# Optimization experiments

Hardware: AMD Instinct MI355X
Metric: run time of the kernel (lower is better)

## Reference

```python
import jax, jax.numpy as jnp
import numpy as np

B, S, H = 8, 2048, 256

def setup_inputs() -> dict:
    key = jax.random.key(0)
    ks = jax.random.split(key, 6)
    scale = 1.0 / np.sqrt(H)
    return {
        "query": jax.random.normal(ks[0], (B, S, H), dtype=jnp.float32),
        "key_in": jax.random.normal(ks[1], (B, S, H), dtype=jnp.float32),
        "value": jax.random.normal(ks[2], (B, S, H), dtype=jnp.float32),
        "Wq": jax.random.uniform(ks[3], (H, H), dtype=jnp.float32, minval=-scale, maxval=scale),
        "Wk": jax.random.uniform(ks[4], (H, H), dtype=jnp.float32, minval=-scale, maxval=scale),
        "Wv": jax.random.uniform(ks[5], (H, H), dtype=jnp.float32, minval=-scale, maxval=scale),
    }

def reference(query, key_in, value, Wq, Wk, Wv):
    # nn.Linear(bias=False): y = x @ W.T
    q = jnp.einsum('bsh,dh->bsd', query, Wq)
    k = jnp.einsum('bsh,dh->bsd', key_in, Wk)
    v = jnp.einsum('bsh,dh->bsd', value, Wv)
    # unscaled attention, exactly as in the torch module
    scores = jnp.einsum('bqd,bkd->bqk', q, k)  # [B, Sq, Skv]
    weights = jax.nn.softmax(scores, axis=-1)
    context = jnp.einsum('bqk,bkd->bqd', weights, v)
    return context
```

## Files before the change

kernel.cpp:

```cpp
#include <hip/hip_runtime.h>
#include <hip/hip_bf16.h>

typedef short short8 __attribute__((ext_vector_type(8)));
typedef _Float16 half8 __attribute__((ext_vector_type(8)));
typedef __fp16 fp16x2 __attribute__((ext_vector_type(2)));
typedef float f32x4  __attribute__((ext_vector_type(4)));
typedef float f32x16 __attribute__((ext_vector_type(16)));

__device__ __forceinline__ unsigned short f2h(float f) {
  _Float16 h = (_Float16)f;
  return __builtin_bit_cast(unsigned short, h);
}
__device__ __forceinline__ half8 as_h8(short8 s) { return __builtin_bit_cast(half8, s); }

__global__ __launch_bounds__(256) void proj_kernel(
    const float* __restrict__ Aq, const float* __restrict__ Bq,
    const float* __restrict__ Ak, const float* __restrict__ Bk,
    const float* __restrict__ Av, const float* __restrict__ Bv,
    short* __restrict__ Cq, short* __restrict__ Ck, short* __restrict__ Cv) {
  __shared__ short At[128][40];
  __shared__ short Bt[128][40];
  const int y = blockIdx.y;
  const float* A  = (y == 0) ? Aq : (y == 1) ? Ak : Av;
  const float* Bm = (y == 0) ? Bq : (y == 1) ? Bk : Bv;
  short* C        = (y == 0) ? Cq : (y == 1) ? Ck : Cv;
  const int mode = (y == 2);
  const float scale = (y == 0) ? 1.44269504f : 1.0f;
  const int x = blockIdx.x;
  const int batch = x & 7, loc = (x >> 3) & 15, half = x >> 7;
  int m0, n0;
  if (!mode) { m0 = (batch * 16 + loc) * 128; n0 = half * 128; }
  else       { m0 = half * 128; n0 = (batch * 16 + loc) * 128; }

  const int t = threadIdx.x;
  const int w = t >> 6, l = t & 63;
  const int wr = (w >> 1) * 64, wc = (w & 1) * 64;
  f32x4 acc[4][4] = {};
  for (int k0 = 0; k0 < 256; k0 += 32) {
    __syncthreads();
    #pragma unroll
    for (int rep = 0; rep < 4; ++rep) {
      int row = (t >> 3) + rep * 32;
      int c4  = (t & 7) * 4;
      float4 va = *(const float4*)(A + (size_t)(m0 + row) * 256 + k0 + c4);
      unsigned long long pa = (unsigned long long)f2h(va.x) |
                              ((unsigned long long)f2h(va.y) << 16) |
                              ((unsigned long long)f2h(va.z) << 32) |
                              ((unsigned long long)f2h(va.w) << 48);
      *(unsigned long long*)&At[row][c4] = pa;
      float4 vb = *(const float4*)(Bm + (size_t)(n0 + row) * 256 + k0 + c4);
      unsigned long long pb = (unsigned long long)f2h(vb.x) |
                              ((unsigned long long)f2h(vb.y) << 16) |
                              ((unsigned long long)f2h(vb.z) << 32) |
                              ((unsigned long long)f2h(vb.w) << 48);
      *(unsigned long long*)&Bt[row][c4] = pb;
    }
    __syncthreads();
    short8 af[4], bf[4];
    #pragma unroll
    for (int i = 0; i < 4; ++i) {
      af[i] = *(const short8*)&At[wr + i * 16 + (l & 15)][(l >> 4) * 8];
      bf[i] = *(const short8*)&Bt[wc + i * 16 + (l & 15)][(l >> 4) * 8];
    }
    #pragma unroll
    for (int i = 0; i < 4; ++i)
      #pragma unroll
      for (int j = 0; j < 4; ++j)
        acc[i][j] = __builtin_amdgcn_mfma_f32_16x16x32_f16(as_h8(af[i]), as_h8(bf[j]),
                                                           acc[i][j], 0, 0, 0);
  }
  #pragma unroll
  for (int i = 0; i < 4; ++i)
    #pragma unroll
    for (int j = 0; j < 4; ++j)
      #pragma unroll
      for (int r = 0; r < 4; ++r) {
        int row = m0 + wr + i * 16 + (l >> 4) * 4 + r;
        int col = n0 + wc + j * 16 + (l & 15);
        size_t idx;
        if (!mode) {
          int b = row >> 11, s = row & 2047;
          int T = s >> 5, ln = s & 31;
          int kf = col >> 4, g = (col >> 3) & 1, jj = col & 7;
          idx = (((size_t)(b * 64 + T) * 16 + kf) * 64 + g * 32 + ln) * 8 + jj;
        } else {
          int b = col >> 11, s = col & 2047;
          int T = s >> 5, k2 = (s >> 4) & 1, g = (s >> 3) & 1, jj = s & 7;
          int db = row >> 5, ln = row & 31;
          idx = ((((size_t)(b * 64 + T) * 2 + k2) * 8 + db) * 64 + g * 32 + ln) * 8 + jj;
        }
        C[idx] = (short)f2h(acc[i][j][r] * scale);
      }
}

__global__ __launch_bounds__(512, 4) void attn_kernel(const short* __restrict__ QP,
                                                      const short* __restrict__ KP,
                                                      const short* __restrict__ VP,
                                                      float* __restrict__ O) {
  __shared__ __align__(16) char arena[16384 + 40960 + 1024 + 1024];
  short* Qlds = (short*)arena;
  short (*Plds)[8][32][40] = (short (*)[8][32][40])(arena + 16384);
  float (*mx_sh)[8] = (float (*)[8])(arena + 16384 + 40960);
  float (*l_sh)[8]  = (float (*)[8])(arena + 16384 + 40960 + 1024);
  float (*tbuf)[32][33] = (float (*)[32][33])arena;

  const int t = threadIdx.x;
  const int w = t >> 6, l = t & 63;
  const int q = l & 31, grp = l >> 5;
  const int sw = ((q >> 3) & 3) << 3;
  const int bid = blockIdx.x;
  const int b = bid & 7;
  const int q0 = (bid >> 3) * 32;
  const size_t bS = (size_t)b * 2048;

  {
    const short* qsrc = QP + ((size_t)(b * 64 + (q0 >> 5)) * 16) * 512;
    *(short8*)&Qlds[t * 8] = *(const short8*)(qsrc + t * 8);
    *(short8*)&Qlds[(t + 512) * 8] = *(const short8*)(qsrc + (t + 512) * 8);
  }
  __syncthreads();

  const short* kptr = KP + (((size_t)(b * 64 + w)) << 13) + l * 8;
  const short* vptr = VP + (((size_t)(b * 64)) << 13) + ((size_t)w << 9) + l * 8;

  f32x16 ot0 = {}, ot1 = {};
  float m = -1e30f, lsum = 0.f;

  for (int it = 0; it < 8; ++it) {
    const short* kb = kptr + ((size_t)it << 16);
    f32x16 st0 = {}, st1 = {};
    __builtin_amdgcn_s_setprio(1);
    #pragma unroll
    for (int kf = 0; kf < 16; kf += 2) {
      short8 a0 = *(const short8*)(kb + kf * 512);
      short8 a1 = *(const short8*)(kb + (kf + 1) * 512);
      short8 qa = *(const short8*)&Qlds[kf * 512 + l * 8];
      short8 qb = *(const short8*)&Qlds[(kf + 1) * 512 + l * 8];
      st0 = __builtin_amdgcn_mfma_f32_32x32x16_f16(as_h8(a0), as_h8(qa), st0, 0, 0, 0);
      st1 = __builtin_amdgcn_mfma_f32_32x32x16_f16(as_h8(a1), as_h8(qb), st1, 0, 0, 0);
    }
    __builtin_amdgcn_s_setprio(0);
    f32x16 st = st0 + st1;

    float a0m = fmaxf(fmaxf(st[0], st[1]), fmaxf(st[2], st[3]));
    float a1m = fmaxf(fmaxf(st[4], st[5]), fmaxf(st[6], st[7]));
    float a2m = fmaxf(fmaxf(st[8], st[9]), fmaxf(st[10], st[11]));
    float a3m = fmaxf(fmaxf(st[12], st[13]), fmaxf(st[14], st[15]));
    float tmax = fmaxf(fmaxf(a0m, a1m), fmaxf(a2m, a3m));
    tmax = fmaxf(tmax, __shfl_xor(tmax, 32, 64));
    if (l < 32) mx_sh[q][w] = tmax;
    __syncthreads();

    f32x4 mA = *(const f32x4*)&mx_sh[q][0];
    f32x4 mB = *(const f32x4*)&mx_sh[q][4];
    float t8 = fmaxf(fmaxf(fmaxf(mA[0], mA[1]), fmaxf(mA[2], mA[3])),
                     fmaxf(fmaxf(mB[0], mB[1]), fmaxf(mB[2], mB[3])));
    bool need = !__all(t8 - m <= 11.544f);
    float mnew = need ? fmaxf(m, t8) : m;
    float corr = exp2f(m - mnew);

    float p[16];
    #pragma unroll
    for (int r = 0; r < 16; ++r) p[r] = exp2f(st[r] - mnew);
    float s0 = (p[0] + p[1]) + (p[2] + p[3]);
    float s1 = (p[4] + p[5]) + (p[6] + p[7]);
    float s2 = (p[8] + p[9]) + (p[10] + p[11]);
    float s3 = (p[12] + p[13]) + (p[14] + p[15]);
    float psum = (s0 + s1) + (s2 + s3);
    psum += __shfl_xor(psum, 32, 64);
    lsum = lsum * corr + psum;
    #pragma unroll
    for (int i = 0; i < 8; ++i) {
      fp16x2 pk = __builtin_amdgcn_cvt_pkrtz(p[2 * i], p[2 * i + 1]);
      int kvb = ((2 * i) & 3) + 8 * (i >> 1) + 4 * grp;
      *(unsigned*)&Plds[it & 1][w][q][kvb ^ sw] = __builtin_bit_cast(unsigned, pk);
    }

    if (it) {
      const short (*P)[32][40] = Plds[(it - 1) & 1];
      const short* vb = vptr + ((size_t)(it - 1) << 16);
      __builtin_amdgcn_s_setprio(1);
      #pragma unroll
      for (int t2 = 0; t2 < 8; ++t2) {
        short8 pb0 = *(const short8*)&P[t2][q][(grp * 8) ^ sw];
        short8 pb1 = *(const short8*)&P[t2][q][(grp * 8 + 16) ^ sw];
        short8 vf0 = *(const short8*)(vb + t2 * 8192);
        short8 vf1 = *(const short8*)(vb + t2 * 8192 + 8 * 512);
        ot0 = __builtin_amdgcn_mfma_f32_32x32x16_f16(as_h8(vf0), as_h8(pb0), ot0, 0, 0, 0);
        ot1 = __builtin_amdgcn_mfma_f32_32x32x16_f16(as_h8(vf1), as_h8(pb1), ot1, 0, 0, 0);
      }
      __builtin_amdgcn_s_setprio(0);
    }
    if (need) { ot0 *= corr; ot1 *= corr; }
    m = mnew;
    __syncthreads();
  }

  {
    const short (*P)[32][40] = Plds[1];
    const short* vb = vptr + ((size_t)7 << 16);
    __builtin_amdgcn_s_setprio(1);
    #pragma unroll
    for (int t2 = 0; t2 < 8; ++t2) {
      short8 pb0 = *(const short8*)&P[t2][q][(grp * 8) ^ sw];
      short8 pb1 = *(const short8*)&P[t2][q][(grp * 8 + 16) ^ sw];
      short8 vf0 = *(const short8*)(vb + t2 * 8192);
      short8 vf1 = *(const short8*)(vb + t2 * 8192 + 8 * 512);
      ot0 = __builtin_amdgcn_mfma_f32_32x32x16_f16(as_h8(vf0), as_h8(pb0), ot0, 0, 0, 0);
      ot1 = __builtin_amdgcn_mfma_f32_32x32x16_f16(as_h8(vf1), as_h8(pb1), ot1, 0, 0, 0);
    }
    __builtin_amdgcn_s_setprio(0);
  }

  if (l < 32) l_sh[q][w] = lsum;
  __syncthreads();
  f32x4 lA = *(const f32x4*)&l_sh[q][0];
  f32x4 lB = *(const f32x4*)&l_sh[q][4];
  float Ltot = ((lA[0] + lA[1]) + (lA[2] + lA[3])) + ((lB[0] + lB[1]) + (lB[2] + lB[3]));
  float invL = 1.0f / Ltot;

  #pragma unroll
  for (int r = 0; r < 16; ++r)
    tbuf[w][(r & 3) + 8 * (r >> 2) + 4 * grp][q] = (ot0[r] + ot1[r]) * invL;
  #pragma unroll
  for (int rr = 0; rr < 16; ++rr) {
    int qq = grp + rr * 2;
    O[(bS + q0 + qq) * 256 + w * 32 + q] = tbuf[w][q][qq];
  }
}

extern "C" void kernel_launch(void* const* d_in, const int* in_sizes, int n_in,
                              void* d_out, int out_size, void* d_ws, size_t ws_size,
                              hipStream_t stream) {
  (void)in_sizes; (void)n_in; (void)out_size; (void)ws_size;
  const float* query  = (const float*)d_in[0];
  const float* key_in = (const float*)d_in[1];
  const float* value  = (const float*)d_in[2];
  const float* Wq     = (const float*)d_in[3];
  const float* Wk     = (const float*)d_in[4];
  const float* Wv     = (const float*)d_in[5];
  float* out = (float*)d_out;

  short* q_ws = (short*)d_ws;
  short* k_ws = q_ws + (size_t)16384 * 256;
  short* v_ws = k_ws + (size_t)16384 * 256;

  dim3 gp(256, 3), ga(512);
  proj_kernel<<<gp, 256, 0, stream>>>(query, Wq, key_in, Wk, Wv, value,
                                      q_ws, k_ws, v_ws);
  attn_kernel<<<ga, 512, 0, stream>>>(q_ws, k_ws, v_ws, out);
}
```

Before: 82.29 us.

## Process two KV tiles per phase with a single P buffer, halving barrier rounds

The attention loop now handles two 256-key tiles per phase, so it runs four phases instead of eight. Each phase computes scores for both tiles, reduces the row max once, and writes both probability tiles into one 16-slab LDS buffer. It then runs a 16-step PV MFMA loop. This replaces the double-buffered scheme, where the PV of the previous tile overlapped the QK of the current one. The goal is fewer block-wide syncs and max reductions per key, at the cost of that QK/PV overlap and of the XOR swizzle on P stores, which may reintroduce LDS bank conflicts. A barrier is added before the final transpose because tbuf now aliases the P buffer.

New measurement: 103.5 us. +25.8%, slower.

```diff
diff --git a/kernel.cpp b/kernel.cpp
--- a/kernel.cpp
+++ b/kernel.cpp
@@ -99,7 +99,7 @@
                                                       float* __restrict__ O) {
   __shared__ __align__(16) char arena[16384 + 40960 + 1024 + 1024];
   short* Qlds = (short*)arena;
-  short (*Plds)[8][32][40] = (short (*)[8][32][40])(arena + 16384);
+  short (*Plds)[32][40] = (short (*)[32][40])(arena + 16384);
   float (*mx_sh)[8] = (float (*)[8])(arena + 16384 + 40960);
   float (*l_sh)[8]  = (float (*)[8])(arena + 16384 + 40960 + 1024);
   float (*tbuf)[32][33] = (float (*)[32][33])arena;
@@ -107,7 +107,6 @@
   const int t = threadIdx.x;
   const int w = t >> 6, l = t & 63;
   const int q = l & 31, grp = l >> 5;
-  const int sw = ((q >> 3) & 3) << 3;
   const int bid = blockIdx.x;
   const int b = bid & 7;
   const int q0 = (bid >> 3) * 32;
@@ -126,27 +125,43 @@
   f32x16 ot0 = {}, ot1 = {};
   float m = -1e30f, lsum = 0.f;
 
-  for (int it = 0; it < 8; ++it) {
-    const short* kb = kptr + ((size_t)it << 16);
-    f32x16 st0 = {}, st1 = {};
+  for (int ph = 0; ph < 4; ++ph) {
+    const short* kb0 = kptr + ((size_t)ph << 17);
+    f32x16 s0a = {}, s1a = {};
     __builtin_amdgcn_s_setprio(1);
     #pragma unroll
     for (int kf = 0; kf < 16; kf += 2) {
-      short8 a0 = *(const short8*)(kb + kf * 512);
-      short8 a1 = *(const short8*)(kb + (kf + 1) * 512);
+      short8 a0 = *(const short8*)(kb0 + kf * 512);
+      short8 a1 = *(const short8*)(kb0 + (kf + 1) * 512);
       short8 qa = *(const short8*)&Qlds[kf * 512 + l * 8];
       short8 qb = *(const short8*)&Qlds[(kf + 1) * 512 + l * 8];
-      st0 = __builtin_amdgcn_mfma_f32_32x32x16_f16(as_h8(a0), as_h8(qa), st0, 0, 0, 0);
-      st1 = __builtin_amdgcn_mfma_f32_32x32x16_f16(as_h8(a1), as_h8(qb), st1, 0, 0, 0);
+      s0a = __builtin_amdgcn_mfma_f32_32x32x16_f16(as_h8(a0), as_h8(qa), s0a, 0, 0, 0);
+      s1a = __builtin_amdgcn_mfma_f32_32x32x16_f16(as_h8(a1), as_h8(qb), s1a, 0, 0, 0);
+    }
+    f32x16 sta = s0a + s1a;
+    const short* kb1 = kb0 + 65536;
+    f32x16 s0b = {}, s1b = {};
+    #pragma unroll
+    for (int kf = 0; kf < 16; kf += 2) {
+      short8 a0 = *(const short8*)(kb1 + kf * 512);
+      short8 a1 = *(const short8*)(kb1 + (kf + 1) * 512);
+      short8 qa = *(const short8*)&Qlds[kf * 512 + l * 8];
+      short8 qb = *(const short8*)&Qlds[(kf + 1) * 512 + l * 8];
+      s0b = __builtin_amdgcn_mfma_f32_32x32x16_f16(as_h8(a0), as_h8(qa), s0b, 0, 0, 0);
+      s1b = __builtin_amdgcn_mfma_f32_32x32x16_f16(as_h8(a1), as_h8(qb), s1b, 0, 0, 0);
     }
     __builtin_amdgcn_s_setprio(0);
-    f32x16 st = st0 + st1;
-
-    float a0m = fmaxf(fmaxf(st[0], st[1]), fmaxf(st[2], st[3]));
-    float a1m = fmaxf(fmaxf(st[4], st[5]), fmaxf(st[6], st[7]));
-    float a2m = fmaxf(fmaxf(st[8], st[9]), fmaxf(st[10], st[11]));
-    float a3m = fmaxf(fmaxf(st[12], st[13]), fmaxf(st[14], st[15]));
-    float tmax = fmaxf(fmaxf(a0m, a1m), fmaxf(a2m, a3m));
+    f32x16 stb = s0b + s1b;
+
+    float xa = fmaxf(fmaxf(fmaxf(sta[0], sta[1]), fmaxf(sta[2], sta[3])),
+                     fmaxf(fmaxf(sta[4], sta[5]), fmaxf(sta[6], sta[7])));
+    float xb = fmaxf(fmaxf(fmaxf(sta[8], sta[9]), fmaxf(sta[10], sta[11])),
+                     fmaxf(fmaxf(sta[12], sta[13]), fmaxf(sta[14], sta[15])));
+    float xc = fmaxf(fmaxf(fmaxf(stb[0], stb[1]), fmaxf(stb[2], stb[3])),
+                     fmaxf(fmaxf(stb[4], stb[5]), fmaxf(stb[6], stb[7])));
+    float xd = fmaxf(fmaxf(fmaxf(stb[8], stb[9]), fmaxf(stb[10], stb[11])),
+                     fmaxf(fmaxf(stb[12], stb[13]), fmaxf(stb[14], stb[15])));
+    float tmax = fmaxf(fmaxf(xa, xb), fmaxf(xc, xd));
     tmax = fmaxf(tmax, __shfl_xor(tmax, 32, 64));
     if (l < 32) mx_sh[q][w] = tmax;
     __syncthreads();
@@ -155,57 +170,55 @@
     f32x4 mB = *(const f32x4*)&mx_sh[q][4];
     float t8 = fmaxf(fmaxf(fmaxf(mA[0], mA[1]), fmaxf(mA[2], mA[3])),
                      fmaxf(fmaxf(mB[0], mB[1]), fmaxf(mB[2], mB[3])));
-    bool need = !__all(t8 - m <= 11.544f);
-    float mnew = need ? fmaxf(m, t8) : m;
-    float corr = exp2f(m - mnew);
-
-    float p[16];
-    #pragma unroll
-    for (int r = 0; r < 16; ++r) p[r] = exp2f(st[r] - mnew);
-    float s0 = (p[0] + p[1]) + (p[2] + p[3]);
-    float s1 = (p[4] + p[5]) + (p[6] + p[7]);
-    float s2 = (p[8] + p[9]) + (p[10] + p[11]);
-    float s3 = (p[12] + p[13]) + (p[14] + p[15]);
-    float psum = (s0 + s1) + (s2 + s3);
+
+    if (!__all(t8 - m <= 11.544f)) {
+      float mnew = fmaxf(m, t8);
+      float corr = exp2f(m - mnew);
+      lsum *= corr;
+      ot0 *= corr;
+      ot1 *= corr;
+      m = mnew;
+    }
+
+    float psum = 0.f;
+    {
+      float p[16];
+      #pragma unroll
+      for (int r = 0; r < 16; ++r) p[r] = exp2f(sta[r] - m);
+      psum += ((p[0]+p[1])+(p[2]+p[3])) + ((p[4]+p[5])+(p[6]+p[7])) +
+              ((p[8]+p[9])+(p[10]+p[11])) + ((p[12]+p[13])+(p[14]+p[15]));
+      #pragma unroll
+      for (int i = 0; i < 8; ++i) {
+        fp16x2 pk = __builtin_amdgcn_cvt_pkrtz(p[2 * i], p[2 * i + 1]);
+        int kvb = ((2 * i) & 3) + 8 * (i >> 1) + 4 * grp;
+        *(unsigned*)&Plds[w][q][kvb] = __builtin_bit_cast(unsigned, pk);
+      }
+    }
+    {
+      float p[16];
+      #pragma unroll
+      for (int r = 0; r < 16; ++r) p[r] = exp2f(stb[r] - m);
+      psum += ((p[0]+p[1])+(p[2]+p[3])) + ((p[4]+p[5])+(p[6]+p[7])) +
+              ((p[8]+p[9])+(p[10]+p[11])) + ((p[12]+p[13])+(p[14]+p[15]));
+      #pragma unroll
+      for (int i = 0; i < 8; ++i) {
+        fp16x2 pk = __builtin_amdgcn_cvt_pkrtz(p[2 * i], p[2 * i + 1]);
+        int kvb = ((2 * i) & 3) + 8 * (i >> 1) + 4 * grp;
+        *(unsigned*)&Plds[w + 8][q][kvb] = __builtin_bit_cast(unsigned, pk);
+      }
+    }
     psum += __shfl_xor(psum, 32, 64);
-    lsum = lsum * corr + psum;
-    #pragma unroll
-    for (int i = 0; i < 8; ++i) {
-      fp16x2 pk = __builtin_amdgcn_cvt_pkrtz(p[2 * i], p[2 * i + 1]);
-      int kvb = ((2 * i) & 3) + 8 * (i >> 1) + 4 * grp;
-      *(unsigned*)&Plds[it & 1][w][q][kvb ^ sw] = __builtin_bit_cast(unsigned, pk);
-    }
-
-    if (it) {
-      const short (*P)[32][40] = Plds[(it - 1) & 1];
-      const short* vb = vptr + ((size_t)(it - 1) << 16);
-      __builtin_amdgcn_s_setprio(1);
-      #pragma unroll
-      for (int t2 = 0; t2 < 8; ++t2) {
-        short8 pb0 = *(const short8*)&P[t2][q][(grp * 8) ^ sw];
-        short8 pb1 = *(const short8*)&P[t2][q][(grp * 8 + 16) ^ sw];
-        short8 vf0 = *(const short8*)(vb + t2 * 8192);
-        short8 vf1 = *(const short8*)(vb + t2 * 8192 + 8 * 512);
-        ot0 = __builtin_amdgcn_mfma_f32_32x32x16_f16(as_h8(vf0), as_h8(pb0), ot0, 0, 0, 0);
-        ot1 = __builtin_amdgcn_mfma_f32_32x32x16_f16(as_h8(vf1), as_h8(pb1), ot1, 0, 0, 0);
-      }
-      __builtin_amdgcn_s_setprio(0);
-    }
-    if (need) { ot0 *= corr; ot1 *= corr; }
-    m = mnew;
-    __syncthreads();
-  }
-
-  {
-    const short (*P)[32][40] = Plds[1];
-    const short* vb = vptr + ((size_t)7 << 16);
+    lsum += psum;
+    __syncthreads();
+
+    const short* vb = vptr + ((size_t)ph << 17);
     __builtin_amdgcn_s_setprio(1);
     #pragma unroll
-    for (int t2 = 0; t2 < 8; ++t2) {
-      short8 pb0 = *(const short8*)&P[t2][q][(grp * 8) ^ sw];
-      short8 pb1 = *(const short8*)&P[t2][q][(grp * 8 + 16) ^ sw];
-      short8 vf0 = *(const short8*)(vb + t2 * 8192);
-      short8 vf1 = *(const short8*)(vb + t2 * 8192 + 8 * 512);
+    for (int s = 0; s < 16; ++s) {
+      short8 pb0 = *(const short8*)&Plds[s][q][grp * 8];
+      short8 pb1 = *(const short8*)&Plds[s][q][16 + grp * 8];
+      short8 vf0 = *(const short8*)(vb + s * 8192);
+      short8 vf1 = *(const short8*)(vb + s * 8192 + 4096);
       ot0 = __builtin_amdgcn_mfma_f32_32x32x16_f16(as_h8(vf0), as_h8(pb0), ot0, 0, 0, 0);
       ot1 = __builtin_amdgcn_mfma_f32_32x32x16_f16(as_h8(vf1), as_h8(pb1), ot1, 0, 0, 0);
     }
@@ -218,6 +231,7 @@
   f32x4 lB = *(const f32x4*)&l_sh[q][4];
   float Ltot = ((lA[0] + lA[1]) + (lA[2] + lA[3])) + ((lB[0] + lB[1]) + (lB[2] + lB[3]));
   float invL = 1.0f / Ltot;
+  __syncthreads();
 
   #pragma unroll
   for (int r = 0; r < 16; ++r)
```
